# Kernel tuning notes

Hardware: AMD Instinct MI355X
Metric: run time of the kernel (lower is better)

The kernel has to match this reference:

```python
import jax, jax.numpy as jnp
import numpy as np


def setup_inputs() -> dict:
    key = jax.random.key(0)
    k1, k2 = jax.random.split(key)
    B, N, K, Q, D = 8, 20, 5, 15, 1024
    embeddings = jax.random.normal(k1, (B, N, K + Q, D), dtype=jnp.float32)
    # scoring Linear(4*D, 1): weight [1, 4D], bias [1] (init_weight fills bias with 0.01)
    weight = jax.random.normal(k2, (1, 4 * D), dtype=jnp.float32) * 0.02
    bias = jnp.full((1,), 0.01, dtype=jnp.float32)
    return {"embeddings": embeddings, "weight": weight, "bias": bias,
            "N": N, "K": K, "Q": Q}


def reference(embeddings, weight, bias, N, K, Q):
    # embeddings: [B, N, K+Q, D]
    B = embeddings.shape[0]
    D = embeddings.shape[-1]
    emb = embeddings.reshape(B, N, K + Q, D)
    support = emb[:, :, :K, :]                       # [B, N, K, D]
    query = emb[:, :, K:, :].reshape(B, N * Q, D)    # [B, NQ, D]
    proto = support.mean(axis=2)                     # [B, N, D]

    # scoring weight over concat [proto, query, |p-q|, p*q] along last dim:
    # logits = p.w0 + q.w1 + |p-q|.w2 + (p*q).w3 + b  -- same math, no 4D concat
    w = weight.reshape(4, D)
    term_p = jnp.einsum('bnd,d->bn', proto, w[0])[:, None, :]      # [B,1,N]
    term_q = jnp.einsum('bqd,d->bq', query, w[1])[:, :, None]      # [B,NQ,1]
    p = proto[:, None, :, :]                                       # [B,1,N,D]
    q = query[:, :, None, :]                                       # [B,NQ,1,D]
    term_abs = jnp.einsum('bqnd,d->bqn', jnp.abs(p - q), w[2])     # [B,NQ,N]
    term_cos = jnp.einsum('bqd,bnd->bqn', query * w[3], proto)     # [B,NQ,N]
    logits = term_p + term_q + term_abs + term_cos + bias[0]
    return logits
```

## Files before the change

kernel.cpp:

```cpp
#include <hip/hip_runtime.h>

#define DCONST 1024
#define KSUP 5
#define NPROTO 20
#define QPER 15
#define SLOTS (KSUP + QPER)

__global__ __launch_bounds__(256) void proto_kernel(
    const float* __restrict__ emb,
    const float* __restrict__ weight,
    float* __restrict__ proto,
    float* __restrict__ term_p)
{
    const int bn  = blockIdx.x;
    const int tid = threadIdx.x;
    const int d0  = tid * 4;

    const float* base = emb + ((size_t)bn * SLOTS) * DCONST + d0;
    float4 s = make_float4(0.f, 0.f, 0.f, 0.f);
#pragma unroll
    for (int k = 0; k < KSUP; ++k) {
        float4 v = *reinterpret_cast<const float4*>(base + (size_t)k * DCONST);
        s.x += v.x; s.y += v.y; s.z += v.z; s.w += v.w;
    }
    const float inv = 1.0f / (float)KSUP;
    s.x *= inv; s.y *= inv; s.z *= inv; s.w *= inv;
    *reinterpret_cast<float4*>(proto + (size_t)bn * DCONST + d0) = s;

    float4 w0 = *reinterpret_cast<const float4*>(weight + d0);
    float part = s.x * w0.x + s.y * w0.y + s.z * w0.z + s.w * w0.w;

    for (int off = 32; off; off >>= 1) part += __shfl_down(part, off, 64);
    __shared__ float red[4];
    const int wid = tid >> 6;
    if ((tid & 63) == 0) red[wid] = part;
    __syncthreads();
    if (tid == 0) term_p[bn] = red[0] + red[1] + red[2] + red[3];
}

__global__ __launch_bounds__(256) void logits_kernel(
    const float* __restrict__ emb,
    const float* __restrict__ weight,
    const float* __restrict__ bias,
    const float* __restrict__ proto,
    const float* __restrict__ term_p,
    float* __restrict__ out,
    int B)
{
    const int tid  = threadIdx.x;
    const int lane = tid & 63;
    const int wid  = tid >> 6;
    const int NQ   = NPROTO * QPER;
    const int blocks_per_b = NQ / 4;
    const int b  = blockIdx.x / blocks_per_b;
    const int qp = (blockIdx.x % blocks_per_b) * 4 + wid;
    const int nsrc = qp / QPER;
    const int qq   = qp % QPER;

    const float* qrow =
        emb + (((size_t)(b * NPROTO + nsrc) * SLOTS) + KSUP + qq) * DCONST;

    float4 q4[4], w2r[4], qw3[4];
#pragma unroll
    for (int j = 0; j < 4; ++j) {
        const int d = j * 256 + lane * 4;
        q4[j]  = *reinterpret_cast<const float4*>(qrow + d);
        w2r[j] = *reinterpret_cast<const float4*>(weight + 2 * DCONST + d);
        float4 w3 = *reinterpret_cast<const float4*>(weight + 3 * DCONST + d);
        qw3[j] = make_float4(q4[j].x * w3.x, q4[j].y * w3.y,
                             q4[j].z * w3.z, q4[j].w * w3.w);
    }

    float tq = 0.f;
#pragma unroll
    for (int j = 0; j < 4; ++j) {
        const int d = j * 256 + lane * 4;
        float4 w1 = *reinterpret_cast<const float4*>(weight + DCONST + d);
        tq += q4[j].x * w1.x + q4[j].y * w1.y + q4[j].z * w1.z + q4[j].w * w1.w;
    }
    for (int off = 32; off; off >>= 1) tq += __shfl_down(tq, off, 64);
    tq = __shfl(tq, 0, 64);
    const float cbase = tq + bias[0];

    float* orow = out + ((size_t)b * NQ + qp) * NPROTO;
    const float* pbase  = proto + (size_t)b * NPROTO * DCONST;
    const float* tpbase = term_p + b * NPROTO;

    for (int n = 0; n < NPROTO; ++n) {
        float acc = 0.f;
#pragma unroll
        for (int j = 0; j < 4; ++j) {
            const int d = j * 256 + lane * 4;
            float4 p = *reinterpret_cast<const float4*>(pbase + (size_t)n * DCONST + d);
            acc += fabsf(p.x - q4[j].x) * w2r[j].x + qw3[j].x * p.x;
            acc += fabsf(p.y - q4[j].y) * w2r[j].y + qw3[j].y * p.y;
            acc += fabsf(p.z - q4[j].z) * w2r[j].z + qw3[j].z * p.z;
            acc += fabsf(p.w - q4[j].w) * w2r[j].w + qw3[j].w * p.w;
        }
        for (int off = 32; off; off >>= 1) acc += __shfl_down(acc, off, 64);
        if (lane == 0) orow[n] = acc + cbase + tpbase[n];
    }
}

extern "C" void kernel_launch(void* const* d_in, const int* in_sizes, int n_in,
                              void* d_out, int out_size, void* d_ws, size_t ws_size,
                              hipStream_t stream) {
    const float* emb    = (const float*)d_in[0];
    const float* weight = (const float*)d_in[1];
    const float* bias   = (const float*)d_in[2];
    float* out = (float*)d_out;

    const int B = in_sizes[0] / (NPROTO * SLOTS * DCONST);

    float* proto  = (float*)d_ws;
    float* term_p = proto + (size_t)B * NPROTO * DCONST;

    proto_kernel<<<B * NPROTO, 256, 0, stream>>>(emb, weight, proto, term_p);

    const int NQ = NPROTO * QPER;
    logits_kernel<<<B * (NQ / 4), 256, 0, stream>>>(emb, weight, bias,
                                                    proto, term_p, out, B);
}
```

Measured before the change: 82.22 us.

## Split prototype loop across two blocks and batch accumulators with coalesced store

The logits kernel now launches twice as many blocks, and each block handles half of the 20 prototypes for its four queries. That shortens the serial loop per block and raises parallelism. The 10 prototype dot products are unrolled into independent accumulators written with explicit FMAs, and each is reduced with xor shuffles. One lane per prototype then writes the result, instead of a serial shuffle reduction and a lane-0 store per prototype. The cost is that each query row and the weight vectors are now loaded twice, and register pressure goes up, which the launch-bounds occupancy hint tries to contain.

```diff
diff --git a/kernel.cpp b/kernel.cpp
--- a/kernel.cpp
+++ b/kernel.cpp
@@ -5,6 +5,8 @@
 #define NPROTO 20
 #define QPER 15
 #define SLOTS (KSUP + QPER)
+#define NQ (NPROTO * QPER)
+#define NHALF (NPROTO / 2)
 
 __global__ __launch_bounds__(256) void proto_kernel(
     const float* __restrict__ emb,
@@ -30,6 +32,7 @@
     float4 w0 = *reinterpret_cast<const float4*>(weight + d0);
     float part = s.x * w0.x + s.y * w0.y + s.z * w0.z + s.w * w0.w;
 
+#pragma unroll
     for (int off = 32; off; off >>= 1) part += __shfl_down(part, off, 64);
     __shared__ float red[4];
     const int wid = tid >> 6;
@@ -38,22 +41,22 @@
     if (tid == 0) term_p[bn] = red[0] + red[1] + red[2] + red[3];
 }
 
-__global__ __launch_bounds__(256) void logits_kernel(
+__global__ __launch_bounds__(256, 4) void logits_kernel(
     const float* __restrict__ emb,
     const float* __restrict__ weight,
     const float* __restrict__ bias,
     const float* __restrict__ proto,
     const float* __restrict__ term_p,
-    float* __restrict__ out,
-    int B)
+    float* __restrict__ out)
 {
     const int tid  = threadIdx.x;
     const int lane = tid & 63;
     const int wid  = tid >> 6;
-    const int NQ   = NPROTO * QPER;
+    const int half = blockIdx.x & 1;
+    const int grp  = blockIdx.x >> 1;
     const int blocks_per_b = NQ / 4;
-    const int b  = blockIdx.x / blocks_per_b;
-    const int qp = (blockIdx.x % blocks_per_b) * 4 + wid;
+    const int b  = grp / blocks_per_b;
+    const int qp = (grp % blocks_per_b) * 4 + wid;
     const int nsrc = qp / QPER;
     const int qq   = qp % QPER;
 
@@ -61,44 +64,61 @@
         emb + (((size_t)(b * NPROTO + nsrc) * SLOTS) + KSUP + qq) * DCONST;
 
     float4 q4[4], w2r[4], qw3[4];
+    float tq = 0.f;
 #pragma unroll
     for (int j = 0; j < 4; ++j) {
         const int d = j * 256 + lane * 4;
         q4[j]  = *reinterpret_cast<const float4*>(qrow + d);
         w2r[j] = *reinterpret_cast<const float4*>(weight + 2 * DCONST + d);
         float4 w3 = *reinterpret_cast<const float4*>(weight + 3 * DCONST + d);
+        float4 w1 = *reinterpret_cast<const float4*>(weight + 1 * DCONST + d);
         qw3[j] = make_float4(q4[j].x * w3.x, q4[j].y * w3.y,
                              q4[j].z * w3.z, q4[j].w * w3.w);
-    }
-
-    float tq = 0.f;
-#pragma unroll
-    for (int j = 0; j < 4; ++j) {
-        const int d = j * 256 + lane * 4;
-        float4 w1 = *reinterpret_cast<const float4*>(weight + DCONST + d);
         tq += q4[j].x * w1.x + q4[j].y * w1.y + q4[j].z * w1.z + q4[j].w * w1.w;
     }
-    for (int off = 32; off; off >>= 1) tq += __shfl_down(tq, off, 64);
-    tq = __shfl(tq, 0, 64);
+#pragma unroll
+    for (int off = 32; off; off >>= 1) tq += __shfl_xor(tq, off, 64);
     const float cbase = tq + bias[0];
 
-    float* orow = out + ((size_t)b * NQ + qp) * NPROTO;
-    const float* pbase  = proto + (size_t)b * NPROTO * DCONST;
-    const float* tpbase = term_p + b * NPROTO;
+    const float* pbase = proto + ((size_t)(b * NPROTO) + half * NHALF) * DCONST;
 
-    for (int n = 0; n < NPROTO; ++n) {
-        float acc = 0.f;
+    float acc[NHALF];
+#pragma unroll
+    for (int n = 0; n < NHALF; ++n) acc[n] = 0.f;
+
+#pragma unroll
+    for (int n = 0; n < NHALF; ++n) {
+        const float* prow = pbase + (size_t)n * DCONST;
 #pragma unroll
         for (int j = 0; j < 4; ++j) {
             const int d = j * 256 + lane * 4;
-            float4 p = *reinterpret_cast<const float4*>(pbase + (size_t)n * DCONST + d);
-            acc += fabsf(p.x - q4[j].x) * w2r[j].x + qw3[j].x * p.x;
-            acc += fabsf(p.y - q4[j].y) * w2r[j].y + qw3[j].y * p.y;
-            acc += fabsf(p.z - q4[j].z) * w2r[j].z + qw3[j].z * p.z;
-            acc += fabsf(p.w - q4[j].w) * w2r[j].w + qw3[j].w * p.w;
+            float4 p = *reinterpret_cast<const float4*>(prow + d);
+            float a = acc[n];
+            a = fmaf(fabsf(p.x - q4[j].x), w2r[j].x, a);
+            a = fmaf(qw3[j].x, p.x, a);
+            a = fmaf(fabsf(p.y - q4[j].y), w2r[j].y, a);
+            a = fmaf(qw3[j].y, p.y, a);
+            a = fmaf(fabsf(p.z - q4[j].z), w2r[j].z, a);
+            a = fmaf(qw3[j].z, p.z, a);
+            a = fmaf(fabsf(p.w - q4[j].w), w2r[j].w, a);
+            a = fmaf(qw3[j].w, p.w, a);
+            acc[n] = a;
         }
-        for (int off = 32; off; off >>= 1) acc += __shfl_down(acc, off, 64);
-        if (lane == 0) orow[n] = acc + cbase + tpbase[n];
+    }
+
+    float myval = 0.f;
+#pragma unroll
+    for (int n = 0; n < NHALF; ++n) {
+        float r = acc[n];
+#pragma unroll
+        for (int off = 32; off; off >>= 1) r += __shfl_xor(r, off, 64);
+        if (lane == n) myval = r;
+    }
+
+    if (lane < NHALF) {
+        const int n = half * NHALF + lane;
+        out[((size_t)b * NQ + qp) * NPROTO + n] =
+            myval + cbase + term_p[b * NPROTO + n];
     }
 }
 
@@ -117,7 +137,6 @@
 
     proto_kernel<<<B * NPROTO, 256, 0, stream>>>(emb, weight, proto, term_p);
 
-    const int NQ = NPROTO * QPER;
-    logits_kernel<<<B * (NQ / 4), 256, 0, stream>>>(emb, weight, bias,
-                                                    proto, term_p, out, B);
+    logits_kernel<<<B * (NQ / 4) * 2, 256, 0, stream>>>(emb, weight, bias,
+                                                        proto, term_p, out);
 }
```

Result: slower. 84.12 us (+2.3%).
